# Optimization experiments

Measured on AMD Instinct MI355X. Metric: run time of the kernel, lower is better.

Reference implementation:

```python
import jax, jax.numpy as jnp
from jax import lax
import numpy as np

B, C, H, W = 8, 128, 256, 256
K_BANK = 4          # num_kernels
KS = 3              # kernel_size
OC = 128            # out_channels


def setup_inputs() -> dict:
    key = jax.random.key(0)
    k1, k2, k3, k4 = jax.random.split(key, 4)
    x = jax.random.normal(k1, (B, C, H, W), dtype=jnp.float32)
    # nn.Parameter(torch.randn(num_kernels, in_channels, 1, ks, ks))
    kernel_bank = jax.random.normal(k2, (K_BANK, C, 1, KS, KS), dtype=jnp.float32)
    # nn.Linear(in_channels, num_kernels)
    attn_w = jax.random.normal(k3, (K_BANK, C), dtype=jnp.float32) * 0.02
    attn_b = jnp.zeros((K_BANK,), dtype=jnp.float32)
    # nn.Conv2d(in_channels, out_channels, 1)
    pw_w = jax.random.normal(k4, (OC, C, 1, 1), dtype=jnp.float32) * 0.05
    pw_b = jnp.zeros((OC,), dtype=jnp.float32)
    return {"x": x, "kernel_bank": kernel_bank, "attn_w": attn_w,
            "attn_b": attn_b, "pw_w": pw_w, "pw_b": pw_b}


def reference(x, kernel_bank, attn_w, attn_b, pw_w, pw_b):
    b, c, h, w = x.shape
    nk, _, _, ks, _ = kernel_bank.shape
    pad = ks // 2
    # GAP -> FC -> softmax attention over kernel bank
    pooled = jnp.mean(x, axis=(2, 3))                          # [B, C]
    attn = jax.nn.softmax(pooled @ attn_w.T + attn_b, axis=1)  # [B, K]
    # per-sample dynamic depthwise kernel: [B, C, ks, ks]
    dyn_kernel = jnp.einsum('bk,kcij->bcij', attn, kernel_bank[:, :, 0])
    # per-sample depthwise conv via grouped conv with B*C groups
    xr = x.reshape(1, b * c, h, w)
    wr = dyn_kernel.reshape(b * c, 1, ks, ks)
    dw = lax.conv_general_dilated(
        xr, wr, window_strides=(1, 1), padding=[(pad, pad), (pad, pad)],
        feature_group_count=b * c,
        dimension_numbers=('NCHW', 'OIHW', 'NCHW'))
    dw = dw.reshape(b, c, h, w)
    # fixed pointwise 1x1 conv
    out = jnp.einsum('bchw,oc->bohw', dw, pw_w[:, :, 0, 0]) + pw_b[None, :, None, None]
    return out
```

## Files before the change

kernel.cpp:

```cpp
#include <hip/hip_runtime.h>
#include <hip/hip_bf16.h>
#include <math.h>

typedef __attribute__((ext_vector_type(8))) short short8;
typedef __attribute__((ext_vector_type(4))) float f32x4;

#define C_IN 128
#define OC_ 128
#define BB 8
#define KBANK 4

__device__ __forceinline__ unsigned short f2bf(float f) {
  union { float f; unsigned int u; } v; v.f = f;
  unsigned int u = v.u;
  unsigned int r = u + 0x7fffu + ((u >> 16) & 1u);
  return (unsigned short)(r >> 16);
}

__global__ void k_pool(const float* __restrict__ x, float* __restrict__ pooled) {
  int plane = blockIdx.x;
  const float4* p = (const float4*)(x + (size_t)plane * 65536);
  float s0 = 0.f, s1 = 0.f, s2 = 0.f, s3 = 0.f;
  for (int i = threadIdx.x; i < 16384; i += 1024) {
    float4 a = p[i];
    float4 b = p[i + 256];
    float4 c = p[i + 512];
    float4 d = p[i + 768];
    s0 += (a.x + a.y) + (a.z + a.w);
    s1 += (b.x + b.y) + (b.z + b.w);
    s2 += (c.x + c.y) + (c.z + c.w);
    s3 += (d.x + d.y) + (d.z + d.w);
  }
  float s = (s0 + s1) + (s2 + s3);
  #pragma unroll
  for (int off = 32; off > 0; off >>= 1) s += __shfl_down(s, off);
  __shared__ float red[4];
  if ((threadIdx.x & 63) == 0) red[threadIdx.x >> 6] = s;
  __syncthreads();
  if (threadIdx.x == 0)
    pooled[plane] = (red[0] + red[1] + red[2] + red[3]) * (1.0f / 65536.0f);
}

__global__ void k_prep(const float* __restrict__ pooled,
                       const float* __restrict__ attn_w,
                       const float* __restrict__ attn_b,
                       const float* __restrict__ bank,
                       const float* __restrict__ pw_w,
                       float* __restrict__ dynk,
                       unsigned short* __restrict__ pwb)
{
  __shared__ float attn_s[BB][KBANK];
  int tid = threadIdx.x;
  {
    int pr = tid >> 3, g = tid & 7;
    int b = pr >> 2, k = pr & 3;
    float s = 0.f;
    #pragma unroll
    for (int j = 0; j < 16; ++j) {
      int c = g * 16 + j;
      s += pooled[b * C_IN + c] * attn_w[k * C_IN + c];
    }
    s += __shfl_xor(s, 1);
    s += __shfl_xor(s, 2);
    s += __shfl_xor(s, 4);
    if (g == 0) attn_s[b][k] = s + attn_b[k];
  }
  __syncthreads();
  if (tid < BB) {
    int b = tid;
    float l0 = attn_s[b][0], l1 = attn_s[b][1], l2 = attn_s[b][2], l3 = attn_s[b][3];
    float m = fmaxf(fmaxf(l0, l1), fmaxf(l2, l3));
    float e0 = expf(l0 - m), e1 = expf(l1 - m), e2 = expf(l2 - m), e3 = expf(l3 - m);
    float inv = 1.0f / (e0 + e1 + e2 + e3);
    attn_s[b][0] = e0 * inv; attn_s[b][1] = e1 * inv;
    attn_s[b][2] = e2 * inv; attn_s[b][3] = e3 * inv;
  }
  __syncthreads();
  for (int i = tid; i < BB * C_IN * 9; i += 256) {
    int b = i / (C_IN * 9);
    int rem = i - b * (C_IN * 9);
    float v = 0.f;
    #pragma unroll
    for (int k = 0; k < KBANK; ++k) v += attn_s[b][k] * bank[k * (C_IN * 9) + rem];
    dynk[i] = v;
  }
  for (int i = tid; i < OC_ * C_IN; i += 256) pwb[i] = f2bf(pw_w[i]);
}

__global__ __launch_bounds__(256, 3) void k_main(
    const float* __restrict__ x,
    const float* __restrict__ dynk,
    const unsigned short* __restrict__ pwb,
    const float* __restrict__ pw_b,
    float* __restrict__ out) {
  constexpr int RS = 18;
  constexpr int PS = 181;
  __shared__ float xs[32 * PS];
  __shared__ unsigned short dws[128 * 40];

  const int b  = blockIdx.z;
  const int h0 = blockIdx.y * 8;
  const int w0 = blockIdx.x * 16;
  const int tid  = threadIdx.x;
  const int wv   = tid >> 6;
  const int lane = tid & 63;
  const int quad = lane >> 4;
  const int l15  = lane & 15;
  const int cl   = tid & 31;
  const int prow = tid >> 5;

  const int c0 = tid >> 3, r0 = tid & 7;
  const int gh0 = h0 - 1 + r0;
  const bool ok0 = (unsigned)gh0 < 256u;
  const float* g0 = x + (((size_t)(b * C_IN + c0)) << 16)
                      + (size_t)(ok0 ? gh0 : 0) * 256 + (w0 - 1);
  float* s0p = xs + c0 * PS + r0 * RS;
  const int c1 = tid >> 1, r1 = 8 + (tid & 1);
  const int gh1 = h0 - 1 + r1;
  const bool ok1 = (unsigned)gh1 < 256u;
  const float* g1 = x + (((size_t)(b * C_IN + c1)) << 16)
                      + (size_t)(ok1 ? gh1 : 0) * 256 + (w0 - 1);
  float* s1p = xs + c1 * PS + r1 * RS;
  const bool has2 = tid < 64;
  const bool wL = (w0 > 0), wR = (w0 < 240);

  short8 afrag[2][4];
  #pragma unroll
  for (int mt = 0; mt < 2; ++mt)
    #pragma unroll
    for (int kc = 0; kc < 4; ++kc) {
      int o = wv * 32 + mt * 16 + l15;
      afrag[mt][kc] = *(const short8*)(pwb + ((size_t)o * C_IN + kc * 32 + quad * 8));
    }

  f32x4 acc[2][8];
  #pragma unroll
  for (int mt = 0; mt < 2; ++mt)
    #pragma unroll
    for (int nt = 0; nt < 8; ++nt)
      acc[mt][nt] = (f32x4){0.f, 0.f, 0.f, 0.f};

  #pragma unroll
  for (int kc = 0; kc < 4; ++kc) {
    __syncthreads();
    {
      float v[18];
      if (ok0) {
        float4 a = *(const float4*)(g0 + 1);
        float4 bq = *(const float4*)(g0 + 5);
        float4 cq = *(const float4*)(g0 + 9);
        float4 dq = *(const float4*)(g0 + 13);
        v[0] = wL ? g0[0] : 0.f;
        v[17] = wR ? g0[17] : 0.f;
        v[1] = a.x; v[2] = a.y; v[3] = a.z; v[4] = a.w;
        v[5] = bq.x; v[6] = bq.y; v[7] = bq.z; v[8] = bq.w;
        v[9] = cq.x; v[10] = cq.y; v[11] = cq.z; v[12] = cq.w;
        v[13] = dq.x; v[14] = dq.y; v[15] = dq.z; v[16] = dq.w;
      } else {
        #pragma unroll
        for (int j = 0; j < 18; ++j) v[j] = 0.f;
      }
      #pragma unroll
      for (int j = 0; j < 18; ++j) s0p[j] = v[j];
      if (has2) {
        float u[18];
        if (ok1) {
          float4 a = *(const float4*)(g1 + 1);
          float4 bq = *(const float4*)(g1 + 5);
          float4 cq = *(const float4*)(g1 + 9);
          float4 dq = *(const float4*)(g1 + 13);
          u[0] = wL ? g1[0] : 0.f;
          u[17] = wR ? g1[17] : 0.f;
          u[1] = a.x; u[2] = a.y; u[3] = a.z; u[4] = a.w;
          u[5] = bq.x; u[6] = bq.y; u[7] = bq.z; u[8] = bq.w;
          u[9] = cq.x; u[10] = cq.y; u[11] = cq.z; u[12] = cq.w;
          u[13] = dq.x; u[14] = dq.y; u[15] = dq.z; u[16] = dq.w;
        } else {
          #pragma unroll
          for (int j = 0; j < 18; ++j) u[j] = 0.f;
        }
        #pragma unroll
        for (int j = 0; j < 18; ++j) s1p[j] = u[j];
      }
      g0 += (size_t)32 << 16;
      g1 += (size_t)32 << 16;
    }
    __syncthreads();
    float k9[9];
    {
      const float* kp = dynk + (size_t)(b * C_IN + kc * 32 + cl) * 9;
      #pragma unroll
      for (int t = 0; t < 9; ++t) k9[t] = kp[t];
    }
    float accd[16];
    #pragma unroll
    for (int col = 0; col < 16; ++col) accd[col] = 0.f;
    const float* xp = &xs[cl * PS + prow * RS];
    #pragma unroll
    for (int i = 0; i < 3; ++i) {
      float xr[18];
      const float* rp = xp + i * RS;
      #pragma unroll
      for (int j = 0; j < 18; ++j) xr[j] = rp[j];
      float cc0 = k9[3 * i], cc1 = k9[3 * i + 1], cc2 = k9[3 * i + 2];
      #pragma unroll
      for (int col = 0; col < 16; ++col)
        accd[col] = fmaf(cc0, xr[col], fmaf(cc1, xr[col + 1], fmaf(cc2, xr[col + 2], accd[col])));
    }
    #pragma unroll
    for (int col = 0; col < 16; ++col)
      dws[(prow * 16 + col) * 40 + cl] = f2bf(accd[col]);
    __syncthreads();
    #pragma unroll
    for (int nt = 0; nt < 8; ++nt) {
      short8 bfrag = *(const short8*)&dws[(nt * 16 + l15) * 40 + quad * 8];
      acc[0][nt] = __builtin_amdgcn_mfma_f32_16x16x32_bf16(afrag[0][kc], bfrag, acc[0][nt], 0, 0, 0);
      acc[1][nt] = __builtin_amdgcn_mfma_f32_16x16x32_bf16(afrag[1][kc], bfrag, acc[1][nt], 0, 0, 0);
    }
  }
  #pragma unroll
  for (int mt = 0; mt < 2; ++mt) {
    #pragma unroll
    for (int r = 0; r < 4; ++r) {
      int o = wv * 32 + mt * 16 + quad * 4 + r;
      float bias = pw_b[o];
      size_t obase = ((size_t)(b * OC_ + o)) << 16;
      #pragma unroll
      for (int nt = 0; nt < 8; ++nt)
        out[obase + ((h0 + nt) << 8) + (w0 + l15)] = acc[mt][nt][r] + bias;
    }
  }
}

extern "C" void kernel_launch(void* const* d_in, const int* in_sizes, int n_in,
                              void* d_out, int out_size, void* d_ws, size_t ws_size,
                              hipStream_t stream) {
  const float* x      = (const float*)d_in[0];
  const float* bank   = (const float*)d_in[1];
  const float* attn_w = (const float*)d_in[2];
  const float* attn_b = (const float*)d_in[3];
  const float* pw_w   = (const float*)d_in[4];
  const float* pw_b   = (const float*)d_in[5];
  float* out = (float*)d_out;

  char* ws = (char*)d_ws;
  float* pooled       = (float*)ws;
  float* dynk         = (float*)(ws + 4096);
  unsigned short* pwb = (unsigned short*)(ws + 4096 + 36864);

  k_pool<<<1024, 256, 0, stream>>>(x, pooled);
  k_prep<<<1, 256, 0, stream>>>(pooled, attn_w, attn_b, bank, pw_w, dynk, pwb);
  dim3 grid(16, 32, 8);
  k_main<<<grid, 256, 0, stream>>>(x, dynk, pwb, pw_b, out);
}
```

Measured before the change: 637.2 us.

## Prefetch next channel chunk into registers, remap grid, stream outputs non-temporally

Global loads of the next 32-channel slab are issued into registers before the depthwise compute of the current slab, so their latency overlaps with compute. The change also spreads halo-row loading across 128 threads instead of 64 and loads the A fragments per chunk instead of keeping them resident, which frees registers. The grid is flattened so the batch index varies fastest, output stores use non-temporal hints, and the pooling loop is restructured with 8 accumulators and larger strides. Holding prefetched values across the compute raises register pressure, which could offset the registers saved on A fragments.

```diff
diff --git a/kernel.cpp b/kernel.cpp
--- a/kernel.cpp
+++ b/kernel.cpp
@@ -17,21 +17,31 @@
   return (unsigned short)(r >> 16);
 }
 
-__global__ void k_pool(const float* __restrict__ x, float* __restrict__ pooled) {
+__global__ __launch_bounds__(256) void k_pool(const float* __restrict__ x,
+                                              float* __restrict__ pooled) {
   int plane = blockIdx.x;
-  const float4* p = (const float4*)(x + (size_t)plane * 65536);
+  const float4* p = (const float4*)(x + ((size_t)plane << 16));
   float s0 = 0.f, s1 = 0.f, s2 = 0.f, s3 = 0.f;
-  for (int i = threadIdx.x; i < 16384; i += 1024) {
-    float4 a = p[i];
-    float4 b = p[i + 256];
-    float4 c = p[i + 512];
-    float4 d = p[i + 768];
-    s0 += (a.x + a.y) + (a.z + a.w);
-    s1 += (b.x + b.y) + (b.z + b.w);
-    s2 += (c.x + c.y) + (c.z + c.w);
-    s3 += (d.x + d.y) + (d.z + d.w);
-  }
-  float s = (s0 + s1) + (s2 + s3);
+  float s4 = 0.f, s5 = 0.f, s6 = 0.f, s7 = 0.f;
+  for (int i = threadIdx.x; i < 2048; i += 256) {
+    float4 a0 = p[i];
+    float4 a1 = p[i + 2048];
+    float4 a2 = p[i + 4096];
+    float4 a3 = p[i + 6144];
+    float4 a4 = p[i + 8192];
+    float4 a5 = p[i + 10240];
+    float4 a6 = p[i + 12288];
+    float4 a7 = p[i + 14336];
+    s0 += (a0.x + a0.y) + (a0.z + a0.w);
+    s1 += (a1.x + a1.y) + (a1.z + a1.w);
+    s2 += (a2.x + a2.y) + (a2.z + a2.w);
+    s3 += (a3.x + a3.y) + (a3.z + a3.w);
+    s4 += (a4.x + a4.y) + (a4.z + a4.w);
+    s5 += (a5.x + a5.y) + (a5.z + a5.w);
+    s6 += (a6.x + a6.y) + (a6.z + a6.w);
+    s7 += (a7.x + a7.y) + (a7.z + a7.w);
+  }
+  float s = ((s0 + s1) + (s2 + s3)) + ((s4 + s5) + (s6 + s7));
   #pragma unroll
   for (int off = 32; off > 0; off >>= 1) s += __shfl_down(s, off);
   __shared__ float red[4];
@@ -87,6 +97,47 @@
   for (int i = tid; i < OC_ * C_IN; i += 256) pwb[i] = f2bf(pw_w[i]);
 }
 
+__device__ __forceinline__ void load18(const float* __restrict__ g, bool ok,
+                                       bool eL, bool eR, float* v) {
+  if (ok) {
+    float4 a = *(const float4*)(g + 1);
+    float4 b = *(const float4*)(g + 5);
+    float4 c = *(const float4*)(g + 9);
+    float4 d = *(const float4*)(g + 13);
+    v[0] = eL ? g[0] : 0.f;
+    v[17] = eR ? g[17] : 0.f;
+    v[1] = a.x; v[2] = a.y; v[3] = a.z; v[4] = a.w;
+    v[5] = b.x; v[6] = b.y; v[7] = b.z; v[8] = b.w;
+    v[9] = c.x; v[10] = c.y; v[11] = c.z; v[12] = c.w;
+    v[13] = d.x; v[14] = d.y; v[15] = d.z; v[16] = d.w;
+  } else {
+    #pragma unroll
+    for (int j = 0; j < 18; ++j) v[j] = 0.f;
+  }
+}
+
+__device__ __forceinline__ void load9(const float* __restrict__ g, bool ok,
+                                      bool eL, bool eR, int hf, float* u) {
+  if (ok) {
+    if (hf == 0) {
+      float4 a = *(const float4*)(g + 1);
+      float4 b = *(const float4*)(g + 5);
+      u[0] = eL ? g[0] : 0.f;
+      u[1] = a.x; u[2] = a.y; u[3] = a.z; u[4] = a.w;
+      u[5] = b.x; u[6] = b.y; u[7] = b.z; u[8] = b.w;
+    } else {
+      float4 a = *(const float4*)(g + 9);
+      float4 b = *(const float4*)(g + 13);
+      u[0] = a.x; u[1] = a.y; u[2] = a.z; u[3] = a.w;
+      u[4] = b.x; u[5] = b.y; u[6] = b.z; u[7] = b.w;
+      u[8] = eR ? g[17] : 0.f;
+    }
+  } else {
+    #pragma unroll
+    for (int j = 0; j < 9; ++j) u[j] = 0.f;
+  }
+}
+
 __global__ __launch_bounds__(256, 3) void k_main(
     const float* __restrict__ x,
     const float* __restrict__ dynk,
@@ -98,9 +149,13 @@
   __shared__ float xs[32 * PS];
   __shared__ unsigned short dws[128 * 40];
 
-  const int b  = blockIdx.z;
-  const int h0 = blockIdx.y * 8;
-  const int w0 = blockIdx.x * 16;
+  const int b  = blockIdx.x & 7;
+  const int t  = blockIdx.x >> 3;
+  const int bx = t & 15;
+  const int by = t >> 4;
+  const int h0 = by * 8;
+  const int w0 = bx * 16;
+
   const int tid  = threadIdx.x;
   const int wv   = tid >> 6;
   const int lane = tid & 63;
@@ -115,23 +170,17 @@
   const float* g0 = x + (((size_t)(b * C_IN + c0)) << 16)
                       + (size_t)(ok0 ? gh0 : 0) * 256 + (w0 - 1);
   float* s0p = xs + c0 * PS + r0 * RS;
-  const int c1 = tid >> 1, r1 = 8 + (tid & 1);
+  const bool has2 = tid < 128;
+  const int c1 = tid >> 2;
+  const int hf = (tid >> 1) & 1;
+  const int r1 = 8 + (tid & 1);
   const int gh1 = h0 - 1 + r1;
   const bool ok1 = (unsigned)gh1 < 256u;
   const float* g1 = x + (((size_t)(b * C_IN + c1)) << 16)
                       + (size_t)(ok1 ? gh1 : 0) * 256 + (w0 - 1);
-  float* s1p = xs + c1 * PS + r1 * RS;
-  const bool has2 = tid < 64;
+  float* s1p = xs + c1 * PS + r1 * RS + hf * 9;
+
   const bool wL = (w0 > 0), wR = (w0 < 240);
-
-  short8 afrag[2][4];
-  #pragma unroll
-  for (int mt = 0; mt < 2; ++mt)
-    #pragma unroll
-    for (int kc = 0; kc < 4; ++kc) {
-      int o = wv * 32 + mt * 16 + l15;
-      afrag[mt][kc] = *(const short8*)(pwb + ((size_t)o * C_IN + kc * 32 + quad * 8));
-    }
 
   f32x4 acc[2][8];
   #pragma unroll
@@ -140,58 +189,34 @@
     for (int nt = 0; nt < 8; ++nt)
       acc[mt][nt] = (f32x4){0.f, 0.f, 0.f, 0.f};
 
+  float vp[18], up[9];
+  load18(g0, ok0, wL, wR, vp);
+  if (has2) load9(g1, ok1, wL, wR, hf, up);
+
   #pragma unroll
   for (int kc = 0; kc < 4; ++kc) {
     __syncthreads();
-    {
-      float v[18];
-      if (ok0) {
-        float4 a = *(const float4*)(g0 + 1);
-        float4 bq = *(const float4*)(g0 + 5);
-        float4 cq = *(const float4*)(g0 + 9);
-        float4 dq = *(const float4*)(g0 + 13);
-        v[0] = wL ? g0[0] : 0.f;
-        v[17] = wR ? g0[17] : 0.f;
-        v[1] = a.x; v[2] = a.y; v[3] = a.z; v[4] = a.w;
-        v[5] = bq.x; v[6] = bq.y; v[7] = bq.z; v[8] = bq.w;
-        v[9] = cq.x; v[10] = cq.y; v[11] = cq.z; v[12] = cq.w;
-        v[13] = dq.x; v[14] = dq.y; v[15] = dq.z; v[16] = dq.w;
-      } else {
-        #pragma unroll
-        for (int j = 0; j < 18; ++j) v[j] = 0.f;
-      }
-      #pragma unroll
-      for (int j = 0; j < 18; ++j) s0p[j] = v[j];
-      if (has2) {
-        float u[18];
-        if (ok1) {
-          float4 a = *(const float4*)(g1 + 1);
-          float4 bq = *(const float4*)(g1 + 5);
-          float4 cq = *(const float4*)(g1 + 9);
-          float4 dq = *(const float4*)(g1 + 13);
-          u[0] = wL ? g1[0] : 0.f;
-          u[17] = wR ? g1[17] : 0.f;
-          u[1] = a.x; u[2] = a.y; u[3] = a.z; u[4] = a.w;
-          u[5] = bq.x; u[6] = bq.y; u[7] = bq.z; u[8] = bq.w;
-          u[9] = cq.x; u[10] = cq.y; u[11] = cq.z; u[12] = cq.w;
-          u[13] = dq.x; u[14] = dq.y; u[15] = dq.z; u[16] = dq.w;
-        } else {
-          #pragma unroll
-          for (int j = 0; j < 18; ++j) u[j] = 0.f;
-        }
-        #pragma unroll
-        for (int j = 0; j < 18; ++j) s1p[j] = u[j];
-      }
+    #pragma unroll
+    for (int j = 0; j < 18; ++j) s0p[j] = vp[j];
+    if (has2) {
+      #pragma unroll
+      for (int j = 0; j < 9; ++j) s1p[j] = up[j];
+    }
+    if (kc < 3) {
       g0 += (size_t)32 << 16;
       g1 += (size_t)32 << 16;
-    }
-    __syncthreads();
+      load18(g0, ok0, wL, wR, vp);
+      if (has2) load9(g1, ok1, wL, wR, hf, up);
+    }
     float k9[9];
     {
       const float* kp = dynk + (size_t)(b * C_IN + kc * 32 + cl) * 9;
       #pragma unroll
-      for (int t = 0; t < 9; ++t) k9[t] = kp[t];
-    }
+      for (int q = 0; q < 9; ++q) k9[q] = kp[q];
+    }
+    short8 af0 = *(const short8*)(pwb + ((size_t)(wv * 32 + l15) * C_IN + kc * 32 + quad * 8));
+    short8 af1 = *(const short8*)(pwb + ((size_t)(wv * 32 + 16 + l15) * C_IN + kc * 32 + quad * 8));
+    __syncthreads();
     float accd[16];
     #pragma unroll
     for (int col = 0; col < 16; ++col) accd[col] = 0.f;
@@ -214,8 +239,8 @@
     #pragma unroll
     for (int nt = 0; nt < 8; ++nt) {
       short8 bfrag = *(const short8*)&dws[(nt * 16 + l15) * 40 + quad * 8];
-      acc[0][nt] = __builtin_amdgcn_mfma_f32_16x16x32_bf16(afrag[0][kc], bfrag, acc[0][nt], 0, 0, 0);
-      acc[1][nt] = __builtin_amdgcn_mfma_f32_16x16x32_bf16(afrag[1][kc], bfrag, acc[1][nt], 0, 0, 0);
+      acc[0][nt] = __builtin_amdgcn_mfma_f32_16x16x32_bf16(af0, bfrag, acc[0][nt], 0, 0, 0);
+      acc[1][nt] = __builtin_amdgcn_mfma_f32_16x16x32_bf16(af1, bfrag, acc[1][nt], 0, 0, 0);
     }
   }
   #pragma unroll
@@ -227,7 +252,8 @@
       size_t obase = ((size_t)(b * OC_ + o)) << 16;
       #pragma unroll
       for (int nt = 0; nt < 8; ++nt)
-        out[obase + ((h0 + nt) << 8) + (w0 + l15)] = acc[mt][nt][r] + bias;
+        __builtin_nontemporal_store(acc[mt][nt][r] + bias,
+                                    &out[obase + ((h0 + nt) << 8) + (w0 + l15)]);
     }
   }
 }
@@ -250,6 +276,5 @@
 
   k_pool<<<1024, 256, 0, stream>>>(x, pooled);
   k_prep<<<1, 256, 0, stream>>>(pooled, attn_w, attn_b, bank, pw_w, dynk, pwb);
-  dim3 grid(16, 32, 8);
-  k_main<<<grid, 256, 0, stream>>>(x, dynk, pwb, pw_b, out);
-}
+  k_main<<<4096, 256, 0, stream>>>(x, dynk, pwb, pw_b, out);
+}
```

Result: slower. 674.5 us (+5.9%).
